# Kernel optimization log

Measured on AMD Instinct MI355X. Metric: run time of the kernel, lower is better.

The kernel has to match this reference:

```python
import jax, jax.numpy as jnp
import numpy as np

B, N, DIN, DOUT = 16384, 32, 128, 256
ITERS = 3
SQUASH_W = 1.0
EPS_SQUASH = 1e-9
EPS_NORM = 1e-12


def setup_inputs() -> dict:
    key = jax.random.key(0)
    k1, k2, k3 = jax.random.split(key, 3)
    embeds = jax.random.normal(k1, (B, N, DIN), dtype=jnp.float32)
    weights = jax.random.normal(k2, (B, N), dtype=jnp.float32)
    # xavier_normal init for Linear weight, zero-ish bias (torch default bias is
    # uniform but value is irrelevant for a correctness baseline; keep it small)
    xav = float(np.sqrt(2.0 / (DIN + DOUT)))
    W = jax.random.normal(k3, (DIN, DOUT), dtype=jnp.float32) * xav
    b = jnp.zeros((DOUT,), dtype=jnp.float32)
    return {"embeds": embeds, "weights": weights, "W": W, "b": b}


def _squash(s):
    # s: [B, D]; squash along the capsule vector dim D (axis=-2 in the original
    # [B,1,1,D,1] layout == last axis here).
    sq = jnp.sum(s * s, axis=-1, keepdims=True)
    scale = sq / (SQUASH_W + sq) / jnp.sqrt(sq + EPS_SQUASH)
    return scale * s


def reference(embeds, weights, W, b):
    # Linear + (eval-mode) dropout identity; no activation (default None)
    x = jnp.einsum("bni,io->bno", embeds, W) + b          # [B, N, DOUT]
    # F.normalize(p=2, dim=-2) over the capsule vector dim
    nrm = jnp.sqrt(jnp.sum(x * x, axis=-1, keepdims=True))
    u_hat = x / jnp.maximum(nrm, EPS_NORM)                 # [B, N, DOUT]
    u_hat_det = jax.lax.stop_gradient(u_hat)

    b_ij = weights[:, :, None]                             # [B, N, 1]
    c_ij = None
    v = None
    for r in range(ITERS):
        c_ij = jax.nn.softmax(b_ij, axis=1) * N            # [B, N, 1]
        s = jnp.sum(c_ij * u_hat, axis=1)                  # [B, DOUT]
        v = _squash(s)                                     # [B, DOUT]
        if r < ITERS - 1:
            # u_hat^T v  -> per-candidate agreement scalar
            agree = jnp.einsum("bnd,bd->bn", u_hat_det, v)
            b_ij = b_ij + agree[:, :, None]
    poses = v                                              # [B, DOUT]
    c_out = c_ij[:, :, 0]                                  # [B, N]
    return (poses, c_out)
```

## Files before the change

kernel.cpp:

```cpp
#include <hip/hip_runtime.h>
#include <hip/hip_bf16.h>

typedef __attribute__((ext_vector_type(8))) __bf16 bf16x8;
typedef __attribute__((ext_vector_type(4))) __bf16 bf16x4;
typedef __attribute__((ext_vector_type(4))) float  f32x4;

#define B_    16384
#define N_    32
#define DIN_  128
#define DOUT_ 256

__global__ void prep_w(const float* __restrict__ W, __bf16* __restrict__ wp) {
    int tid = blockIdx.x * 256 + threadIdx.x;
    int ks = tid >> 10;
    int ot = (tid >> 6) & 15;
    int l  = tid & 63;
    int k0 = ks * 32 + ((l >> 4) << 3);
    int o  = ot * 16 + (l & 15);
    __bf16 v[8];
#pragma unroll
    for (int j = 0; j < 8; ++j) v[j] = (__bf16)W[(size_t)(k0 + j) * DOUT_ + o];
    *reinterpret_cast<bf16x8*>(&wp[(size_t)tid * 8]) = *reinterpret_cast<bf16x8*>(v);
}

__global__ __launch_bounds__(256, 4) void dyr_main(
    const float* __restrict__ embeds, const float* __restrict__ weights,
    const __bf16* __restrict__ wp,    const float* __restrict__ bias,
    float* __restrict__ out)
{
    __shared__ __bf16 elds[32 * 136];
    __shared__ float  red[4][32];
    __shared__ float  agl[4 * 32];
    __shared__ float  bsh[32];
    __shared__ float  rn[32];
    __shared__ float  sqp[4];

    const int tid = threadIdx.x;
    const int w   = tid >> 6;
    const int l   = tid & 63;
    const int col = l & 15;
    const int q   = l >> 4;
    const int b   = blockIdx.x;

    const float4* e4 = reinterpret_cast<const float4*>(embeds + (size_t)b * N_ * DIN_);
#pragma unroll
    for (int p = 0; p < 4; ++p) {
        int fi = p * 256 + tid;
        float4 v = e4[fi];
        int m = fi >> 5;
        int k = (fi & 31) << 2;
        __bf16 pk[4] = { (__bf16)v.x, (__bf16)v.y, (__bf16)v.z, (__bf16)v.w };
        *reinterpret_cast<bf16x4*>(&elds[m * 136 + k]) = *reinterpret_cast<bf16x4*>(pk);
    }
    if (tid < 32) bsh[tid] = weights[(size_t)b * N_ + tid];
    __syncthreads();

    f32x4 acc[2][4];
#pragma unroll
    for (int mt = 0; mt < 2; ++mt)
#pragma unroll
        for (int t = 0; t < 4; ++t) acc[mt][t] = (f32x4){0.f, 0.f, 0.f, 0.f};

    const int aoff0 = col * 136 + (q << 3);
#pragma unroll
    for (int ks = 0; ks < 4; ++ks) {
        bf16x8 a0 = *reinterpret_cast<const bf16x8*>(&elds[aoff0 + ks * 32]);
        bf16x8 a1 = *reinterpret_cast<const bf16x8*>(&elds[aoff0 + 16 * 136 + ks * 32]);
#pragma unroll
        for (int t = 0; t < 4; ++t) {
            bf16x8 bf = *reinterpret_cast<const bf16x8*>(
                &wp[((size_t)((ks * 16) + (w * 4 + t)) * 64 + l) * 8]);
            acc[0][t] = __builtin_amdgcn_mfma_f32_16x16x32_bf16(a0, bf, acc[0][t], 0, 0, 0);
            acc[1][t] = __builtin_amdgcn_mfma_f32_16x16x32_bf16(a1, bf, acc[1][t], 0, 0, 0);
        }
    }

#pragma unroll
    for (int t = 0; t < 4; ++t) {
        float bv = bias[w * 64 + t * 16 + col];
#pragma unroll
        for (int mt = 0; mt < 2; ++mt)
#pragma unroll
            for (int r = 0; r < 4; ++r) acc[mt][t][r] += bv;
    }

#pragma unroll
    for (int mt = 0; mt < 2; ++mt)
#pragma unroll
        for (int r = 0; r < 4; ++r) {
            float p = 0.f;
#pragma unroll
            for (int t = 0; t < 4; ++t) p += acc[mt][t][r] * acc[mt][t][r];
            p += __shfl_xor(p, 1); p += __shfl_xor(p, 2);
            p += __shfl_xor(p, 4); p += __shfl_xor(p, 8);
            if (col == 0) red[w][mt * 16 + q * 4 + r] = p;
        }
    __syncthreads();
    if (tid < 32) {
        float nsq = red[0][tid] + red[1][tid] + red[2][tid] + red[3][tid];
        rn[tid] = 1.0f / fmaxf(sqrtf(nsq), 1e-12f);
    }
    __syncthreads();
#pragma unroll
    for (int mt = 0; mt < 2; ++mt)
#pragma unroll
        for (int r = 0; r < 4; ++r) {
            float s = rn[mt * 16 + q * 4 + r];
#pragma unroll
            for (int t = 0; t < 4; ++t) acc[mt][t][r] *= s;
        }

    float cme = 0.f;
    float vv[4] = {0.f, 0.f, 0.f, 0.f};
    for (int it = 0; it < 3; ++it) {
        float bval = bsh[l & 31];
        float mx = bval;
        mx = fmaxf(mx, __shfl_xor(mx, 16)); mx = fmaxf(mx, __shfl_xor(mx, 8));
        mx = fmaxf(mx, __shfl_xor(mx, 4));  mx = fmaxf(mx, __shfl_xor(mx, 2));
        mx = fmaxf(mx, __shfl_xor(mx, 1));
        float ex = __expf(bval - mx);
        float sm = ex;
        sm += __shfl_xor(sm, 16); sm += __shfl_xor(sm, 8); sm += __shfl_xor(sm, 4);
        sm += __shfl_xor(sm, 2);  sm += __shfl_xor(sm, 1);
        cme = ex * (32.0f / sm);

        float cv[2][4];
#pragma unroll
        for (int mt = 0; mt < 2; ++mt)
#pragma unroll
            for (int r = 0; r < 4; ++r) cv[mt][r] = __shfl(cme, mt * 16 + q * 4 + r);

        float sv[4];
#pragma unroll
        for (int t = 0; t < 4; ++t) {
            float s = 0.f;
#pragma unroll
            for (int mt = 0; mt < 2; ++mt)
#pragma unroll
                for (int r = 0; r < 4; ++r) s += cv[mt][r] * acc[mt][t][r];
            s += __shfl_xor(s, 16); s += __shfl_xor(s, 32);
            sv[t] = s;
        }

        float loc = sv[0]*sv[0] + sv[1]*sv[1] + sv[2]*sv[2] + sv[3]*sv[3];
        loc += __shfl_xor(loc, 1); loc += __shfl_xor(loc, 2);
        loc += __shfl_xor(loc, 4); loc += __shfl_xor(loc, 8);
        if (l == 0) sqp[w] = loc;
        __syncthreads();
        float sq = sqp[0] + sqp[1] + sqp[2] + sqp[3];
        float scale = sq / ((1.0f + sq) * sqrtf(sq + 1e-9f));
#pragma unroll
        for (int t = 0; t < 4; ++t) vv[t] = scale * sv[t];

        if (it < 2) {
#pragma unroll
            for (int mt = 0; mt < 2; ++mt)
#pragma unroll
                for (int r = 0; r < 4; ++r) {
                    float ap = 0.f;
#pragma unroll
                    for (int t = 0; t < 4; ++t) ap += acc[mt][t][r] * vv[t];
                    ap += __shfl_xor(ap, 1); ap += __shfl_xor(ap, 2);
                    ap += __shfl_xor(ap, 4); ap += __shfl_xor(ap, 8);
                    if (col == 0) agl[w * 32 + mt * 16 + q * 4 + r] = ap;
                }
            __syncthreads();
            if (tid < 32) bsh[tid] += agl[tid] + agl[32 + tid] + agl[64 + tid] + agl[96 + tid];
            __syncthreads();
        }
    }

    if (l < 16) {
#pragma unroll
        for (int t = 0; t < 4; ++t)
            out[(size_t)b * DOUT_ + w * 64 + t * 16 + l] = vv[t];
    }
    if (w == 0 && l < 32)
        out[(size_t)B_ * DOUT_ + (size_t)b * N_ + l] = cme;
}

extern "C" void kernel_launch(void* const* d_in, const int* in_sizes, int n_in,
                              void* d_out, int out_size, void* d_ws, size_t ws_size,
                              hipStream_t stream) {
    const float* embeds  = (const float*)d_in[0];
    const float* weights = (const float*)d_in[1];
    const float* W       = (const float*)d_in[2];
    const float* bias    = (const float*)d_in[3];
    float* out = (float*)d_out;
    __bf16* wp = (__bf16*)d_ws;

    prep_w<<<16, 256, 0, stream>>>(W, wp);
    dyr_main<<<B_, 256, 0, stream>>>(embeds, weights, wp, bias, out);
}
```

Before: 440.6 us.

## Route dynamic routing through a Gram matrix computed with split-fp16 MFMA

Each batch element's 32x32 Gram matrix of the un-normalized projections is computed with MFMA, using a hi/lo fp16 split to keep near-fp32 precision. The three routing iterations then run on this small matrix in a single wave, using readlane broadcasts in place of repeated 256-wide reductions and block barriers. The final pose is rebuilt once from the coefficients folded with the inverse norms. The GEMM inputs also switch from bf16 to fp16. This trades the per-iteration cross-wave reductions for extra MFMA work, about 35KB more LDS (which may cut occupancy), and a serial single-wave section.

```diff
diff --git a/kernel.cpp b/kernel.cpp
--- a/kernel.cpp
+++ b/kernel.cpp
@@ -1,8 +1,8 @@
 #include <hip/hip_runtime.h>
-#include <hip/hip_bf16.h>
-
-typedef __attribute__((ext_vector_type(8))) __bf16 bf16x8;
-typedef __attribute__((ext_vector_type(4))) __bf16 bf16x4;
+
+typedef _Float16 f16;
+typedef __attribute__((ext_vector_type(8))) _Float16 f16x8;
+typedef __attribute__((ext_vector_type(4))) _Float16 f16x4;
 typedef __attribute__((ext_vector_type(4))) float  f32x4;
 
 #define B_    16384
@@ -10,30 +10,45 @@
 #define DIN_  128
 #define DOUT_ 256
 
-__global__ void prep_w(const float* __restrict__ W, __bf16* __restrict__ wp) {
+__device__ __forceinline__ float rdlane(float v, int lane) {
+    return __uint_as_float(__builtin_amdgcn_readlane(__float_as_uint(v), lane));
+}
+__device__ __forceinline__ float red32(float v) {
+    v += __shfl_xor(v, 1); v += __shfl_xor(v, 2); v += __shfl_xor(v, 4);
+    v += __shfl_xor(v, 8); v += __shfl_xor(v, 16);
+    return v;
+}
+__device__ __forceinline__ int xidx(int n, int o) {
+    return n * 272 + (o ^ ((n & 7) << 3));
+}
+
+__global__ void prep_w(const float* __restrict__ W, f16* __restrict__ wp) {
     int tid = blockIdx.x * 256 + threadIdx.x;
     int ks = tid >> 10;
     int ot = (tid >> 6) & 15;
     int l  = tid & 63;
     int k0 = ks * 32 + ((l >> 4) << 3);
     int o  = ot * 16 + (l & 15);
-    __bf16 v[8];
-#pragma unroll
-    for (int j = 0; j < 8; ++j) v[j] = (__bf16)W[(size_t)(k0 + j) * DOUT_ + o];
-    *reinterpret_cast<bf16x8*>(&wp[(size_t)tid * 8]) = *reinterpret_cast<bf16x8*>(v);
-}
+    f16 v[8];
+#pragma unroll
+    for (int j = 0; j < 8; ++j) v[j] = (f16)W[(size_t)(k0 + j) * DOUT_ + o];
+    *reinterpret_cast<f16x8*>(&wp[(size_t)tid * 8]) = *reinterpret_cast<f16x8*>(v);
+}
+
+#define PLANE_ 17408
 
 __global__ __launch_bounds__(256, 4) void dyr_main(
     const float* __restrict__ embeds, const float* __restrict__ weights,
-    const __bf16* __restrict__ wp,    const float* __restrict__ bias,
+    const f16* __restrict__ wp,       const float* __restrict__ bias,
     float* __restrict__ out)
 {
-    __shared__ __bf16 elds[32 * 136];
-    __shared__ float  red[4][32];
-    __shared__ float  agl[4 * 32];
-    __shared__ float  bsh[32];
-    __shared__ float  rn[32];
-    __shared__ float  sqp[4];
+    __shared__ __align__(16) char pool[39584];
+    f16*   elds = reinterpret_cast<f16*>(pool);
+    f16*   xh   = reinterpret_cast<f16*>(pool);
+    f16*   xe   = reinterpret_cast<f16*>(pool + PLANE_);
+    float* glds = reinterpret_cast<float*>(pool + 2 * PLANE_);
+    float* cpls = reinterpret_cast<float*>(pool + 2 * PLANE_ + 4624);
+    float* scls = cpls + 32;
 
     const int tid = threadIdx.x;
     const int w   = tid >> 6;
@@ -41,6 +56,9 @@
     const int col = l & 15;
     const int q   = l >> 4;
     const int b   = blockIdx.x;
+    const int n0  = l & 31;
+
+    float bval = (w == 0) ? weights[(size_t)b * N_ + n0] : 0.f;
 
     const float4* e4 = reinterpret_cast<const float4*>(embeds + (size_t)b * N_ * DIN_);
 #pragma unroll
@@ -49,10 +67,9 @@
         float4 v = e4[fi];
         int m = fi >> 5;
         int k = (fi & 31) << 2;
-        __bf16 pk[4] = { (__bf16)v.x, (__bf16)v.y, (__bf16)v.z, (__bf16)v.w };
-        *reinterpret_cast<bf16x4*>(&elds[m * 136 + k]) = *reinterpret_cast<bf16x4*>(pk);
-    }
-    if (tid < 32) bsh[tid] = weights[(size_t)b * N_ + tid];
+        f16 pk[4] = { (f16)v.x, (f16)v.y, (f16)v.z, (f16)v.w };
+        *reinterpret_cast<f16x4*>(&elds[m * 136 + k]) = *reinterpret_cast<f16x4*>(pk);
+    }
     __syncthreads();
 
     f32x4 acc[2][4];
@@ -64,17 +81,16 @@
     const int aoff0 = col * 136 + (q << 3);
 #pragma unroll
     for (int ks = 0; ks < 4; ++ks) {
-        bf16x8 a0 = *reinterpret_cast<const bf16x8*>(&elds[aoff0 + ks * 32]);
-        bf16x8 a1 = *reinterpret_cast<const bf16x8*>(&elds[aoff0 + 16 * 136 + ks * 32]);
+        f16x8 a0 = *reinterpret_cast<const f16x8*>(&elds[aoff0 + ks * 32]);
+        f16x8 a1 = *reinterpret_cast<const f16x8*>(&elds[aoff0 + 16 * 136 + ks * 32]);
 #pragma unroll
         for (int t = 0; t < 4; ++t) {
-            bf16x8 bf = *reinterpret_cast<const bf16x8*>(
+            f16x8 bf = *reinterpret_cast<const f16x8*>(
                 &wp[((size_t)((ks * 16) + (w * 4 + t)) * 64 + l) * 8]);
-            acc[0][t] = __builtin_amdgcn_mfma_f32_16x16x32_bf16(a0, bf, acc[0][t], 0, 0, 0);
-            acc[1][t] = __builtin_amdgcn_mfma_f32_16x16x32_bf16(a1, bf, acc[1][t], 0, 0, 0);
-        }
-    }
-
+            acc[0][t] = __builtin_amdgcn_mfma_f32_16x16x32_f16(a0, bf, acc[0][t], 0, 0, 0);
+            acc[1][t] = __builtin_amdgcn_mfma_f32_16x16x32_f16(a1, bf, acc[1][t], 0, 0, 0);
+        }
+    }
 #pragma unroll
     for (int t = 0; t < 4; ++t) {
         float bv = bias[w * 64 + t * 16 + col];
@@ -83,100 +99,111 @@
 #pragma unroll
             for (int r = 0; r < 4; ++r) acc[mt][t][r] += bv;
     }
+    __syncthreads();
 
 #pragma unroll
     for (int mt = 0; mt < 2; ++mt)
 #pragma unroll
-        for (int r = 0; r < 4; ++r) {
-            float p = 0.f;
-#pragma unroll
-            for (int t = 0; t < 4; ++t) p += acc[mt][t][r] * acc[mt][t][r];
-            p += __shfl_xor(p, 1); p += __shfl_xor(p, 2);
-            p += __shfl_xor(p, 4); p += __shfl_xor(p, 8);
-            if (col == 0) red[w][mt * 16 + q * 4 + r] = p;
-        }
-    __syncthreads();
-    if (tid < 32) {
-        float nsq = red[0][tid] + red[1][tid] + red[2][tid] + red[3][tid];
-        rn[tid] = 1.0f / fmaxf(sqrtf(nsq), 1e-12f);
-    }
-    __syncthreads();
-#pragma unroll
-    for (int mt = 0; mt < 2; ++mt)
-#pragma unroll
-        for (int r = 0; r < 4; ++r) {
-            float s = rn[mt * 16 + q * 4 + r];
-#pragma unroll
-            for (int t = 0; t < 4; ++t) acc[mt][t][r] *= s;
-        }
-
-    float cme = 0.f;
-    float vv[4] = {0.f, 0.f, 0.f, 0.f};
-    for (int it = 0; it < 3; ++it) {
-        float bval = bsh[l & 31];
-        float mx = bval;
-        mx = fmaxf(mx, __shfl_xor(mx, 16)); mx = fmaxf(mx, __shfl_xor(mx, 8));
-        mx = fmaxf(mx, __shfl_xor(mx, 4));  mx = fmaxf(mx, __shfl_xor(mx, 2));
-        mx = fmaxf(mx, __shfl_xor(mx, 1));
-        float ex = __expf(bval - mx);
-        float sm = ex;
-        sm += __shfl_xor(sm, 16); sm += __shfl_xor(sm, 8); sm += __shfl_xor(sm, 4);
-        sm += __shfl_xor(sm, 2);  sm += __shfl_xor(sm, 1);
-        cme = ex * (32.0f / sm);
-
+        for (int t = 0; t < 4; ++t) {
+            int o = w * 64 + t * 16 + col;
+#pragma unroll
+            for (int r = 0; r < 4; ++r) {
+                float xv = acc[mt][t][r];
+                f16 h = (f16)xv;
+                f16 e = (f16)(xv - (float)h);
+                int idx = xidx(mt * 16 + q * 4 + r, o);
+                xh[idx] = h;
+                xe[idx] = e;
+            }
+        }
+    __syncthreads();
+
+    {
+        const int mi = w >> 1, ni = w & 1;
+        f32x4 gacc = (f32x4){0.f, 0.f, 0.f, 0.f};
+#pragma unroll
+        for (int ks = 0; ks < 8; ++ks) {
+            int ra = xidx(mi * 16 + col, ks * 32 + (q << 3));
+            f16x8 ha = *reinterpret_cast<const f16x8*>(&xh[ra]);
+            f16x8 ea = *reinterpret_cast<const f16x8*>(&xe[ra]);
+            f16x8 hb = ha, eb = ea;
+            if (mi != ni) {
+                int rb = xidx(ni * 16 + col, ks * 32 + (q << 3));
+                hb = *reinterpret_cast<const f16x8*>(&xh[rb]);
+                eb = *reinterpret_cast<const f16x8*>(&xe[rb]);
+            }
+            gacc = __builtin_amdgcn_mfma_f32_16x16x32_f16(ha, hb, gacc, 0, 0, 0);
+            gacc = __builtin_amdgcn_mfma_f32_16x16x32_f16(ha, eb, gacc, 0, 0, 0);
+            gacc = __builtin_amdgcn_mfma_f32_16x16x32_f16(ea, hb, gacc, 0, 0, 0);
+        }
+#pragma unroll
+        for (int r = 0; r < 4; ++r)
+            glds[(mi * 16 + q * 4 + r) * 36 + ni * 16 + col] = gacc[r];
+    }
+    __syncthreads();
+
+    float cval = 0.f, scale = 0.f, rn = 0.f;
+    if (w == 0) {
+        float dv = glds[n0 * 36 + n0];
+        rn = rsqrtf(fmaxf(dv, 1e-24f));
+
+        float g[32];
+#pragma unroll
+        for (int j8 = 0; j8 < 8; ++j8) {
+            f32x4 gv = *reinterpret_cast<const f32x4*>(&glds[n0 * 36 + j8 * 4]);
+#pragma unroll
+            for (int r = 0; r < 4; ++r) g[j8 * 4 + r] = gv[r] * rn;
+        }
+#pragma unroll
+        for (int j = 0; j < 32; ++j) g[j] *= rdlane(rn, j);
+
+        for (int it = 0; it < 3; ++it) {
+            float mx = bval;
+            mx = fmaxf(mx, __shfl_xor(mx, 1));  mx = fmaxf(mx, __shfl_xor(mx, 2));
+            mx = fmaxf(mx, __shfl_xor(mx, 4));  mx = fmaxf(mx, __shfl_xor(mx, 8));
+            mx = fmaxf(mx, __shfl_xor(mx, 16));
+            float ex = __expf(bval - mx);
+            float sm = red32(ex);
+            cval = ex * (32.0f / sm);
+            float t0 = 0.f, t1 = 0.f;
+#pragma unroll
+            for (int j = 0; j < 32; j += 2) {
+                t0 = fmaf(g[j],     rdlane(cval, j),     t0);
+                t1 = fmaf(g[j + 1], rdlane(cval, j + 1), t1);
+            }
+            float t = t0 + t1;
+            float sq = red32(cval * t);
+            scale = sq / ((1.0f + sq) * sqrtf(sq + 1e-9f));
+            if (it < 2) bval = fmaf(scale, t, bval);
+        }
+
+        if (l < 32) {
+            cpls[l] = cval * rn;
+            out[(size_t)B_ * DOUT_ + (size_t)b * N_ + l] = cval;
+        }
+        if (l == 0) *scls = scale;
+    }
+    __syncthreads();
+
+    {
+        float sc = *scls;
         float cv[2][4];
 #pragma unroll
         for (int mt = 0; mt < 2; ++mt)
 #pragma unroll
-            for (int r = 0; r < 4; ++r) cv[mt][r] = __shfl(cme, mt * 16 + q * 4 + r);
-
-        float sv[4];
+            for (int r = 0; r < 4; ++r) cv[mt][r] = cpls[mt * 16 + q * 4 + r];
 #pragma unroll
         for (int t = 0; t < 4; ++t) {
             float s = 0.f;
 #pragma unroll
             for (int mt = 0; mt < 2; ++mt)
 #pragma unroll
-                for (int r = 0; r < 4; ++r) s += cv[mt][r] * acc[mt][t][r];
-            s += __shfl_xor(s, 16); s += __shfl_xor(s, 32);
-            sv[t] = s;
-        }
-
-        float loc = sv[0]*sv[0] + sv[1]*sv[1] + sv[2]*sv[2] + sv[3]*sv[3];
-        loc += __shfl_xor(loc, 1); loc += __shfl_xor(loc, 2);
-        loc += __shfl_xor(loc, 4); loc += __shfl_xor(loc, 8);
-        if (l == 0) sqp[w] = loc;
-        __syncthreads();
-        float sq = sqp[0] + sqp[1] + sqp[2] + sqp[3];
-        float scale = sq / ((1.0f + sq) * sqrtf(sq + 1e-9f));
-#pragma unroll
-        for (int t = 0; t < 4; ++t) vv[t] = scale * sv[t];
-
-        if (it < 2) {
-#pragma unroll
-            for (int mt = 0; mt < 2; ++mt)
-#pragma unroll
-                for (int r = 0; r < 4; ++r) {
-                    float ap = 0.f;
-#pragma unroll
-                    for (int t = 0; t < 4; ++t) ap += acc[mt][t][r] * vv[t];
-                    ap += __shfl_xor(ap, 1); ap += __shfl_xor(ap, 2);
-                    ap += __shfl_xor(ap, 4); ap += __shfl_xor(ap, 8);
-                    if (col == 0) agl[w * 32 + mt * 16 + q * 4 + r] = ap;
-                }
-            __syncthreads();
-            if (tid < 32) bsh[tid] += agl[tid] + agl[32 + tid] + agl[64 + tid] + agl[96 + tid];
-            __syncthreads();
-        }
-    }
-
-    if (l < 16) {
-#pragma unroll
-        for (int t = 0; t < 4; ++t)
-            out[(size_t)b * DOUT_ + w * 64 + t * 16 + l] = vv[t];
-    }
-    if (w == 0 && l < 32)
-        out[(size_t)B_ * DOUT_ + (size_t)b * N_ + l] = cme;
+                for (int r = 0; r < 4; ++r) s = fmaf(cv[mt][r], acc[mt][t][r], s);
+            s += __shfl_xor(s, 16);
+            s += __shfl_xor(s, 32);
+            if (l < 16) out[(size_t)b * DOUT_ + w * 64 + t * 16 + l] = sc * s;
+        }
+    }
 }
 
 extern "C" void kernel_launch(void* const* d_in, const int* in_sizes, int n_in,
@@ -187,7 +214,7 @@
     const float* W       = (const float*)d_in[2];
     const float* bias    = (const float*)d_in[3];
     float* out = (float*)d_out;
-    __bf16* wp = (__bf16*)d_ws;
+    f16* wp = (f16*)d_ws;
 
     prep_w<<<16, 256, 0, stream>>>(W, wp);
     dyr_main<<<B_, 256, 0, stream>>>(embeds, weights, wp, bias, out);
```

Result: no change. 432.3 us (-1.9%).
